# Kernel tuning notes

Measured on AMD Instinct MI355X. Metric: run time of the kernel, lower is better.

Reference implementation:

```python
import jax, jax.numpy as jnp
import numpy as np

TEMPERATURE = 16.0  # sqrt(d_k) with d_k = 256
MASK_FILL = -1e9


def setup_inputs() -> dict:
    key = jax.random.key(0)
    k1, k2, k3, k4, k5 = jax.random.split(key, 5)
    B, N, M, D, DV = 8, 4096, 2048, 256, 256
    q = jax.random.normal(k1, (B, N, D), dtype=jnp.float32)
    k = jax.random.normal(k2, (B, M, D), dtype=jnp.float32)
    v = jax.random.normal(k3, (B, M, DV), dtype=jnp.float32)
    orginal_attention = jax.random.normal(k4, (B, N, M), dtype=jnp.float32)
    mask = jax.random.randint(k5, (B, N, M), 0, 2).astype(jnp.int32)
    feature = 1  # truthy -> no permute of orginal_attention
    return {"q": q, "k": k, "v": v, "orginal_attention": orginal_attention,
            "mask": mask, "feature": feature}


def reference(q, k, v, orginal_attention, mask, feature):
    # attn = (q / T) @ k^T  -> [B, N, M]
    attn = jnp.einsum('bnd,bmd->bnm', q / TEMPERATURE, k)
    attn = jnp.where(mask == 0, MASK_FILL, attn)
    oa = orginal_attention if feature else jnp.transpose(orginal_attention, (0, 2, 1))
    oa = jax.nn.softmax(oa, axis=-1)
    # dropout is identity in eval mode (training=False)
    attn = jax.nn.softmax(attn, axis=-1) + oa
    output = jnp.einsum('bnm,bmv->bnv', attn, v)  # [B, N, DV]
    return output, attn
```

## Files before the change

kernel.cpp:

```cpp
#include <hip/hip_runtime.h>
#include <hip/hip_bf16.h>

typedef __bf16 bf16;
typedef __attribute__((ext_vector_type(4))) __bf16 bf16x4;
typedef __attribute__((ext_vector_type(8))) __bf16 bf16x8;
typedef __attribute__((ext_vector_type(4))) float floatx4;

#define BB 8
#define NN 4096
#define MM 2048
#define DD 256
#define DV 256

__global__ __launch_bounds__(256) void vtrans_kernel(const float* __restrict__ v,
                                                     bf16* __restrict__ vT) {
    const int b  = blockIdx.z;
    const int m0 = blockIdx.y * 64;
    const int d0 = blockIdx.x * 64;
    __shared__ float Ts[64][65];
    const int t  = threadIdx.x;
    const int cf = t & 15;
    const int r  = t >> 4;

    const float* vb = v + ((size_t)b * MM + m0) * DV + d0;
    for (int p = 0; p < 4; ++p) {
        int row = p * 16 + r;
        float4 x = *(const float4*)(vb + (size_t)row * DV + cf * 4);
        Ts[row][cf * 4 + 0] = x.x;
        Ts[row][cf * 4 + 1] = x.y;
        Ts[row][cf * 4 + 2] = x.z;
        Ts[row][cf * 4 + 3] = x.w;
    }
    __syncthreads();
    bf16* ob = vT + ((size_t)b * DV + d0) * MM + m0;
    for (int p = 0; p < 4; ++p) {
        int dv = p * 16 + r;
        bf16x4 w;
        for (int i = 0; i < 4; ++i) w[i] = (bf16)Ts[cf * 4 + i][dv];
        *(bf16x4*)(ob + (size_t)dv * MM + cf * 4) = w;
    }
}

__global__ __launch_bounds__(256) void qk_kernel(const float* __restrict__ q,
                                                 const float* __restrict__ k,
                                                 float* __restrict__ S) {
    const int b  = blockIdx.z;
    const int n0 = blockIdx.y * 128;
    const int m0 = blockIdx.x * 128;

    __shared__ bf16 As[128][72];
    __shared__ bf16 Bs[128][72];

    const int tid  = threadIdx.x;
    const int lane = tid & 63;
    const int wave = tid >> 6;
    const int wr   = (wave & 1) * 64;
    const int wc   = (wave >> 1) * 64;
    const int l15  = lane & 15;
    const int quad = lane >> 4;

    floatx4 acc[4][4] = {};

    const float* qb = q + ((size_t)b * NN + n0) * DD;
    const float* kb = k + ((size_t)b * MM + m0) * DD;

    const int cf = tid & 15;
    const int rr = tid >> 4;

    for (int k0 = 0; k0 < DD; k0 += 64) {
        __syncthreads();
        for (int p = 0; p < 8; ++p) {
            int row = p * 16 + rr;
            float4 aq = *(const float4*)(qb + (size_t)row * DD + k0 + cf * 4);
            float4 bk = *(const float4*)(kb + (size_t)row * DD + k0 + cf * 4);
            bf16x4 wa, wb;
            wa[0] = (bf16)(aq.x * 0.0625f);
            wa[1] = (bf16)(aq.y * 0.0625f);
            wa[2] = (bf16)(aq.z * 0.0625f);
            wa[3] = (bf16)(aq.w * 0.0625f);
            wb[0] = (bf16)bk.x;
            wb[1] = (bf16)bk.y;
            wb[2] = (bf16)bk.z;
            wb[3] = (bf16)bk.w;
            *(bf16x4*)&As[row][cf * 4] = wa;
            *(bf16x4*)&Bs[row][cf * 4] = wb;
        }
        __syncthreads();
        for (int kk = 0; kk < 64; kk += 32) {
            bf16x8 af[4], bfv[4];
            for (int i = 0; i < 4; ++i)
                af[i] = *(const bf16x8*)&As[wr + i * 16 + l15][kk + quad * 8];
            for (int j = 0; j < 4; ++j)
                bfv[j] = *(const bf16x8*)&Bs[wc + j * 16 + l15][kk + quad * 8];
            for (int i = 0; i < 4; ++i)
                for (int j = 0; j < 4; ++j)
                    acc[i][j] = __builtin_amdgcn_mfma_f32_16x16x32_bf16(
                        af[i], bfv[j], acc[i][j], 0, 0, 0);
        }
    }

    float* Sb = S + ((size_t)b * NN + n0) * MM + m0;
    for (int i = 0; i < 4; ++i)
        for (int j = 0; j < 4; ++j) {
            int gc = wc + j * 16 + l15;
            for (int r = 0; r < 4; ++r) {
                int gr = wr + i * 16 + quad * 4 + r;
                Sb[(size_t)gr * MM + gc] = acc[i][j][r];
            }
        }
}

__global__ __launch_bounds__(256) void softmax_add_kernel(const float* __restrict__ oa,
                                                          const int* __restrict__ mask,
                                                          float* __restrict__ attn) {
    const size_t base = (size_t)blockIdx.x * MM;
    const int t    = threadIdx.x;
    const int lane = t & 63;
    const int wv   = t >> 6;

    __shared__ float redS[4], redO[4];

    float s[8], o[8];
    for (int c = 0; c < 2; ++c) {
        float4 s4 = *(const float4*)(attn + base + c * 1024 + t * 4);
        int4   m4 = *(const int4*)(mask + base + c * 1024 + t * 4);
        float4 o4 = *(const float4*)(oa + base + c * 1024 + t * 4);
        s[c * 4 + 0] = m4.x ? s4.x : -1e9f;
        s[c * 4 + 1] = m4.y ? s4.y : -1e9f;
        s[c * 4 + 2] = m4.z ? s4.z : -1e9f;
        s[c * 4 + 3] = m4.w ? s4.w : -1e9f;
        o[c * 4 + 0] = o4.x;
        o[c * 4 + 1] = o4.y;
        o[c * 4 + 2] = o4.z;
        o[c * 4 + 3] = o4.w;
    }

    float mxs = s[0], mxo = o[0];
    for (int i = 1; i < 8; ++i) {
        mxs = fmaxf(mxs, s[i]);
        mxo = fmaxf(mxo, o[i]);
    }
    for (int off = 32; off >= 1; off >>= 1) {
        mxs = fmaxf(mxs, __shfl_xor(mxs, off, 64));
        mxo = fmaxf(mxo, __shfl_xor(mxo, off, 64));
    }
    if (lane == 0) { redS[wv] = mxs; redO[wv] = mxo; }
    __syncthreads();
    mxs = fmaxf(fmaxf(redS[0], redS[1]), fmaxf(redS[2], redS[3]));
    mxo = fmaxf(fmaxf(redO[0], redO[1]), fmaxf(redO[2], redO[3]));
    __syncthreads();

    float sums = 0.f, sumo = 0.f;
    for (int i = 0; i < 8; ++i) {
        s[i] = __expf(s[i] - mxs);
        o[i] = __expf(o[i] - mxo);
        sums += s[i];
        sumo += o[i];
    }
    for (int off = 32; off >= 1; off >>= 1) {
        sums += __shfl_xor(sums, off, 64);
        sumo += __shfl_xor(sumo, off, 64);
    }
    if (lane == 0) { redS[wv] = sums; redO[wv] = sumo; }
    __syncthreads();
    sums = redS[0] + redS[1] + redS[2] + redS[3];
    sumo = redO[0] + redO[1] + redO[2] + redO[3];

    const float invs = 1.0f / sums;
    const float invo = 1.0f / sumo;
    for (int c = 0; c < 2; ++c) {
        float4 w;
        w.x = s[c * 4 + 0] * invs + o[c * 4 + 0] * invo;
        w.y = s[c * 4 + 1] * invs + o[c * 4 + 1] * invo;
        w.z = s[c * 4 + 2] * invs + o[c * 4 + 2] * invo;
        w.w = s[c * 4 + 3] * invs + o[c * 4 + 3] * invo;
        *(float4*)(attn + base + c * 1024 + t * 4) = w;
    }
}

__global__ __launch_bounds__(256) void pv_kernel(const float* __restrict__ attn,
                                                 const bf16* __restrict__ vT,
                                                 float* __restrict__ out) {
    const int b  = blockIdx.z;
    const int n0 = blockIdx.y * 128;
    const int d0 = blockIdx.x * 128;

    __shared__ bf16 As[128][72];
    __shared__ bf16 Bs[128][72];

    const int tid  = threadIdx.x;
    const int lane = tid & 63;
    const int wave = tid >> 6;
    const int wr   = (wave & 1) * 64;
    const int wc   = (wave >> 1) * 64;
    const int l15  = lane & 15;
    const int quad = lane >> 4;

    floatx4 acc[4][4] = {};

    const float* ab  = attn + ((size_t)b * NN + n0) * MM;
    const bf16*  vtb = vT + ((size_t)b * DV + d0) * MM;

    const int cf  = tid & 15;
    const int rr  = tid >> 4;
    const int seg = tid & 1;
    const int vr  = tid >> 1;

    for (int k0 = 0; k0 < MM; k0 += 64) {
        __syncthreads();
        for (int p = 0; p < 8; ++p) {
            int row = p * 16 + rr;
            float4 a4 = *(const float4*)(ab + (size_t)row * MM + k0 + cf * 4);
            bf16x4 w;
            w[0] = (bf16)a4.x;
            w[1] = (bf16)a4.y;
            w[2] = (bf16)a4.z;
            w[3] = (bf16)a4.w;
            *(bf16x4*)&As[row][cf * 4] = w;
        }
        {
            const bf16* src = vtb + (size_t)vr * MM + k0 + seg * 32;
            for (int h = 0; h < 4; ++h) {
                bf16x8 w = *(const bf16x8*)(src + h * 8);
                *(bf16x8*)&Bs[vr][seg * 32 + h * 8] = w;
            }
        }
        __syncthreads();
        for (int kk = 0; kk < 64; kk += 32) {
            bf16x8 af[4], bfv[4];
            for (int i = 0; i < 4; ++i)
                af[i] = *(const bf16x8*)&As[wr + i * 16 + l15][kk + quad * 8];
            for (int j = 0; j < 4; ++j)
                bfv[j] = *(const bf16x8*)&Bs[wc + j * 16 + l15][kk + quad * 8];
            for (int i = 0; i < 4; ++i)
                for (int j = 0; j < 4; ++j)
                    acc[i][j] = __builtin_amdgcn_mfma_f32_16x16x32_bf16(
                        af[i], bfv[j], acc[i][j], 0, 0, 0);
        }
    }

    float* ob = out + ((size_t)b * NN + n0) * DV + d0;
    for (int i = 0; i < 4; ++i)
        for (int j = 0; j < 4; ++j) {
            int gc = wc + j * 16 + l15;
            for (int r = 0; r < 4; ++r) {
                int gr = wr + i * 16 + quad * 4 + r;
                ob[(size_t)gr * DV + gc] = acc[i][j][r];
            }
        }
}

extern "C" void kernel_launch(void* const* d_in, const int* in_sizes, int n_in,
                              void* d_out, int out_size, void* d_ws, size_t ws_size,
                              hipStream_t stream) {
    const float* q    = (const float*)d_in[0];
    const float* k    = (const float*)d_in[1];
    const float* v    = (const float*)d_in[2];
    const float* oa   = (const float*)d_in[3];
    const int*   mask = (const int*)d_in[4];

    float* out  = (float*)d_out;
    float* attn = out + (size_t)BB * NN * DV;
    bf16*  vT   = (bf16*)d_ws;

    vtrans_kernel<<<dim3(DV / 64, MM / 64, BB), 256, 0, stream>>>(v, vT);
    qk_kernel<<<dim3(MM / 128, NN / 128, BB), 256, 0, stream>>>(q, k, attn);
    softmax_add_kernel<<<BB * NN, 256, 0, stream>>>(oa, mask, attn);
    pv_kernel<<<dim3(DV / 128, NN / 128, BB), 256, 0, stream>>>(attn, vT, out);
}
```

Baseline: 911.5 us.

## Pre-convert Q/K to bf16, async LDS loads, wave-per-row softmax, wider PV tiles

Adds conversion kernels that cast Q (pre-scaled by 1/16) and K to bf16 in workspace, then a new QK kernel that uses global_load_lds async copies into unpadded LDS tiles. Softmax now assigns one wave per row, removing shared-memory reductions and block barriers. The PV kernel covers the full 256-wide DV per block with 64-row tiles and async V loads, so each attention tile is read and converted only once. The fast QK path depends on workspace size, and the unpadded LDS layout may cause bank conflicts.

```diff
diff --git a/kernel.cpp b/kernel.cpp
--- a/kernel.cpp
+++ b/kernel.cpp
@@ -11,6 +11,12 @@
 #define MM 2048
 #define DD 256
 #define DV 256
+
+__device__ __forceinline__ void async_copy16(const void* g, void* l) {
+    __builtin_amdgcn_global_load_lds(
+        (const __attribute__((address_space(1))) unsigned int*)g,
+        (__attribute__((address_space(3))) unsigned int*)l, 16, 0, 0);
+}
 
 __global__ __launch_bounds__(256) void vtrans_kernel(const float* __restrict__ v,
                                                      bf16* __restrict__ vT) {
@@ -39,6 +45,79 @@
         for (int i = 0; i < 4; ++i) w[i] = (bf16)Ts[cf * 4 + i][dv];
         *(bf16x4*)(ob + (size_t)dv * MM + cf * 4) = w;
     }
+}
+
+__global__ __launch_bounds__(256) void conv_kernel(const float* __restrict__ src,
+                                                   bf16* __restrict__ dst,
+                                                   float scale) {
+    size_t i = ((size_t)blockIdx.x * 256 + threadIdx.x) * 8;
+    float4 a = *(const float4*)(src + i);
+    float4 b = *(const float4*)(src + i + 4);
+    bf16x8 w;
+    w[0] = (bf16)(a.x * scale); w[1] = (bf16)(a.y * scale);
+    w[2] = (bf16)(a.z * scale); w[3] = (bf16)(a.w * scale);
+    w[4] = (bf16)(b.x * scale); w[5] = (bf16)(b.y * scale);
+    w[6] = (bf16)(b.z * scale); w[7] = (bf16)(b.w * scale);
+    *(bf16x8*)(dst + i) = w;
+}
+
+__global__ __launch_bounds__(256) void qk_fast_kernel(const bf16* __restrict__ qbf,
+                                                      const bf16* __restrict__ kbf,
+                                                      float* __restrict__ S) {
+    const int b  = blockIdx.z;
+    const int n0 = blockIdx.y * 128;
+    const int m0 = blockIdx.x * 128;
+
+    __shared__ bf16 As[128 * 64];
+    __shared__ bf16 Bs[128 * 64];
+
+    const int tid  = threadIdx.x;
+    const int lane = tid & 63;
+    const int wave = tid >> 6;
+    const int wr   = (wave & 1) * 64;
+    const int wc   = (wave >> 1) * 64;
+    const int l15  = lane & 15;
+    const int quad = lane >> 4;
+
+    floatx4 acc[4][4] = {};
+
+    const bf16* qb = qbf + ((size_t)b * NN + n0) * DD;
+    const bf16* kb = kbf + ((size_t)b * MM + m0) * DD;
+
+    const int lrow = lane >> 3;
+    const int lcol = (lane & 7) * 8;
+
+    for (int k0 = 0; k0 < DD; k0 += 64) {
+        __syncthreads();
+        for (int p = 0; p < 4; ++p) {
+            int seg = wave * 4 + p;
+            int row = seg * 8 + lrow;
+            async_copy16(qb + (size_t)row * DD + k0 + lcol, &As[seg * 512]);
+            async_copy16(kb + (size_t)row * DD + k0 + lcol, &Bs[seg * 512]);
+        }
+        __syncthreads();
+        for (int kk = 0; kk < 64; kk += 32) {
+            bf16x8 af[4], bfv[4];
+            for (int i = 0; i < 4; ++i)
+                af[i] = *(const bf16x8*)&As[(wr + i * 16 + l15) * 64 + kk + quad * 8];
+            for (int j = 0; j < 4; ++j)
+                bfv[j] = *(const bf16x8*)&Bs[(wc + j * 16 + l15) * 64 + kk + quad * 8];
+            for (int i = 0; i < 4; ++i)
+                for (int j = 0; j < 4; ++j)
+                    acc[i][j] = __builtin_amdgcn_mfma_f32_16x16x32_bf16(
+                        af[i], bfv[j], acc[i][j], 0, 0, 0);
+        }
+    }
+
+    float* Sb = S + ((size_t)b * NN + n0) * MM + m0;
+    for (int i = 0; i < 4; ++i)
+        for (int j = 0; j < 4; ++j) {
+            int gc = wc + j * 16 + l15;
+            for (int r = 0; r < 4; ++r) {
+                int gr = wr + i * 16 + quad * 4 + r;
+                Sb[(size_t)gr * MM + gc] = acc[i][j][r];
+            }
+        }
 }
 
 __global__ __launch_bounds__(256) void qk_kernel(const float* __restrict__ q,
@@ -113,18 +192,17 @@
 __global__ __launch_bounds__(256) void softmax_add_kernel(const float* __restrict__ oa,
                                                           const int* __restrict__ mask,
                                                           float* __restrict__ attn) {
-    const size_t base = (size_t)blockIdx.x * MM;
-    const int t    = threadIdx.x;
-    const int lane = t & 63;
-    const int wv   = t >> 6;
-
-    __shared__ float redS[4], redO[4];
-
-    float s[8], o[8];
-    for (int c = 0; c < 2; ++c) {
-        float4 s4 = *(const float4*)(attn + base + c * 1024 + t * 4);
-        int4   m4 = *(const int4*)(mask + base + c * 1024 + t * 4);
-        float4 o4 = *(const float4*)(oa + base + c * 1024 + t * 4);
+    const int lane = threadIdx.x & 63;
+    const int wv   = threadIdx.x >> 6;
+    const size_t base = ((size_t)blockIdx.x * 4 + wv) * MM;
+
+    float s[32], o[32];
+#pragma unroll
+    for (int c = 0; c < 8; ++c) {
+        const size_t off = base + c * 256 + lane * 4;
+        float4 s4 = *(const float4*)(attn + off);
+        int4   m4 = *(const int4*)(mask + off);
+        float4 o4 = *(const float4*)(oa + off);
         s[c * 4 + 0] = m4.x ? s4.x : -1e9f;
         s[c * 4 + 1] = m4.y ? s4.y : -1e9f;
         s[c * 4 + 2] = m4.z ? s4.z : -1e9f;
@@ -136,79 +214,73 @@
     }
 
     float mxs = s[0], mxo = o[0];
-    for (int i = 1; i < 8; ++i) {
+#pragma unroll
+    for (int i = 1; i < 32; ++i) {
         mxs = fmaxf(mxs, s[i]);
         mxo = fmaxf(mxo, o[i]);
     }
+#pragma unroll
     for (int off = 32; off >= 1; off >>= 1) {
         mxs = fmaxf(mxs, __shfl_xor(mxs, off, 64));
         mxo = fmaxf(mxo, __shfl_xor(mxo, off, 64));
     }
-    if (lane == 0) { redS[wv] = mxs; redO[wv] = mxo; }
-    __syncthreads();
-    mxs = fmaxf(fmaxf(redS[0], redS[1]), fmaxf(redS[2], redS[3]));
-    mxo = fmaxf(fmaxf(redO[0], redO[1]), fmaxf(redO[2], redO[3]));
-    __syncthreads();
 
     float sums = 0.f, sumo = 0.f;
-    for (int i = 0; i < 8; ++i) {
+#pragma unroll
+    for (int i = 0; i < 32; ++i) {
         s[i] = __expf(s[i] - mxs);
         o[i] = __expf(o[i] - mxo);
         sums += s[i];
         sumo += o[i];
     }
+#pragma unroll
     for (int off = 32; off >= 1; off >>= 1) {
         sums += __shfl_xor(sums, off, 64);
         sumo += __shfl_xor(sumo, off, 64);
     }
-    if (lane == 0) { redS[wv] = sums; redO[wv] = sumo; }
-    __syncthreads();
-    sums = redS[0] + redS[1] + redS[2] + redS[3];
-    sumo = redO[0] + redO[1] + redO[2] + redO[3];
 
     const float invs = 1.0f / sums;
     const float invo = 1.0f / sumo;
-    for (int c = 0; c < 2; ++c) {
+#pragma unroll
+    for (int c = 0; c < 8; ++c) {
         float4 w;
         w.x = s[c * 4 + 0] * invs + o[c * 4 + 0] * invo;
         w.y = s[c * 4 + 1] * invs + o[c * 4 + 1] * invo;
         w.z = s[c * 4 + 2] * invs + o[c * 4 + 2] * invo;
         w.w = s[c * 4 + 3] * invs + o[c * 4 + 3] * invo;
-        *(float4*)(attn + base + c * 1024 + t * 4) = w;
+        *(float4*)(attn + base + c * 256 + lane * 4) = w;
     }
 }
 
 __global__ __launch_bounds__(256) void pv_kernel(const float* __restrict__ attn,
                                                  const bf16* __restrict__ vT,
                                                  float* __restrict__ out) {
-    const int b  = blockIdx.z;
-    const int n0 = blockIdx.y * 128;
-    const int d0 = blockIdx.x * 128;
-
-    __shared__ bf16 As[128][72];
-    __shared__ bf16 Bs[128][72];
+    const int b  = blockIdx.y;
+    const int n0 = blockIdx.x * 64;
+
+    __shared__ bf16 As[64][72];
+    __shared__ bf16 Bs[256 * 64];
 
     const int tid  = threadIdx.x;
     const int lane = tid & 63;
     const int wave = tid >> 6;
-    const int wr   = (wave & 1) * 64;
-    const int wc   = (wave >> 1) * 64;
+    const int wc   = wave * 64;
     const int l15  = lane & 15;
     const int quad = lane >> 4;
 
     floatx4 acc[4][4] = {};
 
     const float* ab  = attn + ((size_t)b * NN + n0) * MM;
-    const bf16*  vtb = vT + ((size_t)b * DV + d0) * MM;
-
-    const int cf  = tid & 15;
-    const int rr  = tid >> 4;
-    const int seg = tid & 1;
-    const int vr  = tid >> 1;
+    const bf16*  vtb = vT + (size_t)b * DV * MM;
+
+    const int cf   = tid & 15;
+    const int rr   = tid >> 4;
+    const int lrow = lane >> 3;
+    const int lcol = (lane & 7) * 8;
 
     for (int k0 = 0; k0 < MM; k0 += 64) {
         __syncthreads();
-        for (int p = 0; p < 8; ++p) {
+        for (int p = 0; p < 4; ++p) {
             int row = p * 16 + rr;
             float4 a4 = *(const float4*)(ab + (size_t)row * MM + k0 + cf * 4);
             bf16x4 w;
@@ -218,20 +290,18 @@
             w[3] = (bf16)a4.w;
             *(bf16x4*)&As[row][cf * 4] = w;
         }
-        {
-            const bf16* src = vtb + (size_t)vr * MM + k0 + seg * 32;
-            for (int h = 0; h < 4; ++h) {
-                bf16x8 w = *(const bf16x8*)(src + h * 8);
-                *(bf16x8*)&Bs[vr][seg * 32 + h * 8] = w;
-            }
+        for (int p = 0; p < 8; ++p) {
+            int seg = wave * 8 + p;
+            int dvr = seg * 8 + lrow;
+            async_copy16(vtb + (size_t)dvr * MM + k0 + lcol, &Bs[seg * 512]);
         }
         __syncthreads();
         for (int kk = 0; kk < 64; kk += 32) {
             bf16x8 af[4], bfv[4];
             for (int i = 0; i < 4; ++i)
-                af[i] = *(const bf16x8*)&As[wr + i * 16 + l15][kk + quad * 8];
+                af[i] = *(const bf16x8*)&As[i * 16 + l15][kk + quad * 8];
             for (int j = 0; j < 4; ++j)
-                bfv[j] = *(const bf16x8*)&Bs[wc + j * 16 + l15][kk + quad * 8];
+                bfv[j] = *(const bf16x8*)&Bs[(wc + j * 16 + l15) * 64 + kk + quad * 8];
             for (int i = 0; i < 4; ++i)
                 for (int j = 0; j < 4; ++j)
                     acc[i][j] = __builtin_amdgcn_mfma_f32_16x16x32_bf16(
@@ -239,12 +309,12 @@
         }
     }
 
-    float* ob = out + ((size_t)b * NN + n0) * DV + d0;
+    float* ob = out + ((size_t)b * NN + n0) * DV;
     for (int i = 0; i < 4; ++i)
         for (int j = 0; j < 4; ++j) {
             int gc = wc + j * 16 + l15;
             for (int r = 0; r < 4; ++r) {
-                int gr = wr + i * 16 + quad * 4 + r;
+                int gr = i * 16 + quad * 4 + r;
                 ob[(size_t)gr * DV + gc] = acc[i][j][r];
             }
         }
@@ -261,10 +331,20 @@
 
     float* out  = (float*)d_out;
     float* attn = out + (size_t)BB * NN * DV;
-    bf16*  vT   = (bf16*)d_ws;
+
+    bf16* vT  = (bf16*)d_ws;
+    bf16* qbf = (bf16*)((char*)d_ws + (size_t)8 * 1024 * 1024);
+    bf16* kbf = (bf16*)((char*)d_ws + (size_t)24 * 1024 * 1024);
+    const bool fast = ws_size >= (size_t)32 * 1024 * 1024;
 
     vtrans_kernel<<<dim3(DV / 64, MM / 64, BB), 256, 0, stream>>>(v, vT);
-    qk_kernel<<<dim3(MM / 128, NN / 128, BB), 256, 0, stream>>>(q, k, attn);
-    softmax_add_kernel<<<BB * NN, 256, 0, stream>>>(oa, mask, attn);
-    pv_kernel<<<dim3(DV / 128, NN / 128, BB), 256, 0, stream>>>(attn, vT, out);
-}
+    if (fast) {
+        conv_kernel<<<(BB * NN * DD / 8 + 255) / 256, 256, 0, stream>>>(q, qbf, 0.0625f);
+        conv_kernel<<<(BB * MM * DD / 8 + 255) / 256, 256, 0, stream>>>(k, kbf, 1.0f);
+        qk_fast_kernel<<<dim3(MM / 128, NN / 128, BB), 256, 0, stream>>>(qbf, kbf, attn);
+    } else {
+        qk_kernel<<<dim3(MM / 128, NN / 128, BB), 256, 0, stream>>>(q, k, attn);
+    }
+    softmax_add_kernel<<<BB * NN / 4, 256, 0, stream>>>(oa, mask, attn);
+    pv_kernel<<<dim3(NN / 64, BB), 256, 0, stream>>>(attn, vT, out);
+}
```

Measured after the change: 872.0 us. 1.05x faster.
